# Optimization experiments

Hardware: AMD Instinct MI355X
Metric: run time of the kernel (lower is better)

## Reference

```python
import jax, jax.numpy as jnp
import numpy as np
import math

BH, L, D = 128, 1024, 64  # batch*heads, maxLen, head_dim
MASK_VALUE = -1000000.0


def setup_inputs() -> dict:
    key = jax.random.key(0)
    kq, kk, kv, kl = jax.random.split(key, 4)
    return {
        "queries": jax.random.normal(kq, (BH, L, D), dtype=jnp.float32),
        "keys": jax.random.normal(kk, (BH, L, D), dtype=jnp.float32),
        "values": jax.random.normal(kv, (BH, L, D), dtype=jnp.float32),
        "valid_lens": jax.random.randint(kl, (BH,), 0, L, dtype=jnp.int32),
    }


def reference(queries, keys, values, valid_lens):
    d = queries.shape[-1]
    # scores: [BH, Lq, Lk]
    scores = jnp.einsum("bqd,bkd->bqk", queries, keys) / math.sqrt(d)
    # key-padding mask: position k valid iff k < valid_len[b]
    mask = jnp.arange(scores.shape[-1])[None, None, :] < valid_lens[:, None, None]
    scores = jnp.where(mask, scores, MASK_VALUE)
    attn = jax.nn.softmax(scores, axis=-1)
    # dropout is identity at inference (Keras Dropout, training=False)
    return jnp.einsum("bqk,bkd->bqd", attn, values)
```

## Files before the change

### kernel.cpp

```cpp
#include <hip/hip_runtime.h>
#include <hip/hip_bf16.h>

#define BH 128
#define L 1024
#define D 64
#define MASK_VALUE -1000000.0f
#define KVBLK 64
#define M0 12.0f

typedef __attribute__((ext_vector_type(8))) __bf16 bf16x8;
typedef __attribute__((ext_vector_type(4))) float f32x4;
typedef __attribute__((ext_vector_type(4))) unsigned int u32x4;

__device__ __forceinline__ unsigned short f2bf(float f) {
    __bf16 h = (__bf16)f;
    return __builtin_bit_cast(unsigned short, h);
}

__device__ __forceinline__ unsigned cvt_pk(float lo, float hi) {
    unsigned r;
    asm("v_cvt_pk_bf16_f32 %0, %1, %2" : "=v"(r) : "v"(lo), "v"(hi));
    return r;
}

__device__ __forceinline__ float exp2_asm(float x) {
    float r; asm("v_exp_f32 %0, %1" : "=v"(r) : "v"(x)); return r;
}

__device__ __forceinline__ f32x4 mfma16(bf16x8 a, bf16x8 b, f32x4 c) {
    return __builtin_amdgcn_mfma_f32_16x16x32_bf16(a, b, c, 0, 0, 0);
}

__device__ __forceinline__ bf16x8 ldsfrag(const unsigned char* base, int row, int colbytes) {
    const u32x4* p = (const u32x4*)(base + row * 128 + (colbytes ^ ((row & 7) << 4)));
    return __builtin_bit_cast(bf16x8, *p);
}

__device__ __forceinline__ int sigma_k(int k) {
    return (k & 0x23) | ((k & 0x0C) << 1) | ((k & 0x10) >> 2);
}

__device__ __forceinline__ int nkt_of(int valid) {
    return (valid == 0) ? (L / KVBLK) : ((valid + KVBLK - 1) >> 6);
}

__global__ void sort_heads(const int* __restrict__ vlen, int* __restrict__ perm) {
    const int j  = threadIdx.x;
    const int nk = nkt_of(vlen[j]);
    int r = 0;
    for (int i = 0; i < BH; ++i) {
        const int nki = nkt_of(vlen[i]);
        if (nki > nk || (nki == nk && i < j)) ++r;
    }
    perm[r] = j;
}

__global__ __launch_bounds__(512)
void attn_kernel(const float* __restrict__ Q, const float* __restrict__ K,
                 const float* __restrict__ V, const int* __restrict__ vlen,
                 const int* __restrict__ perm, float* __restrict__ Out) {
    __shared__ __align__(16) unsigned char Kl[2][64 * 128];
    __shared__ __align__(16) unsigned char Vl[2][64 * 128];

    const int tid  = threadIdx.x;
    const int lane = tid & 63;
    const int wid  = tid >> 6;

    const int bid  = blockIdx.x;
    const int xcd  = bid & 7;
    const int slot = bid >> 3;
    const int c    = slot & 31;
    const int rr   = slot >> 5;
    const int idx  = (rr & 1) ? (rr * 32 + 31 - c) : (rr * 32 + c);
    const int l    = idx >> 3;
    const int qt   = idx & 7;
    const int head = perm[(l << 3) | xcd];

    const int valid = vlen[head];
    const int nkt   = nkt_of(valid);
    const float MASKV = (valid == 0) ? -M0 : MASK_VALUE;

    const float* Qh = Q + (size_t)head * L * D;
    const float* Kh = K + (size_t)head * L * D;
    const float* Vh = V + (size_t)head * L * D;
    float*       Oh = Out + (size_t)head * L * D;

    const int qrow0 = qt * 128 + wid * 16;
    const int q16   = lane & 15;
    const int hi    = lane >> 4;
    const int c8    = hi * 8;

    const float QSCALE = 0.125f * 1.44269504088896f;
    bf16x8 qf[2];
#pragma unroll
    for (int kk = 0; kk < 2; ++kk) {
        const float* qp = Qh + (qrow0 + q16) * D + kk * 32 + c8;
        f32x4 a = *(const f32x4*)qp;
        f32x4 b = *(const f32x4*)(qp + 4);
        u32x4 w;
        w[0] = cvt_pk(a[0] * QSCALE, a[1] * QSCALE);
        w[1] = cvt_pk(a[2] * QSCALE, a[3] * QSCALE);
        w[2] = cvt_pk(b[0] * QSCALE, b[1] * QSCALE);
        w[3] = cvt_pk(b[2] * QSCALE, b[3] * QSCALE);
        qf[kk] = __builtin_bit_cast(bf16x8, w);
    }

    const int skr = tid >> 3;
    const int skc = (tid & 7) * 8;
    const int svk2 = (tid & 31) * 2;
    const int svd4 = (tid >> 5) * 4;
    const int svcb = sigma_k(svk2) * 2;

    f32x4 rk0, rk1;
    f32x4 rva, rvb;

    auto load_regs = [&](int kt) {
        const float* kp = Kh + (size_t)(kt * KVBLK + skr) * D + skc;
        rk0 = *(const f32x4*)kp;
        rk1 = *(const f32x4*)(kp + 4);
        const float* vp = Vh + (size_t)(kt * KVBLK + svk2) * D + svd4;
        rva = *(const f32x4*)vp;
        rvb = *(const f32x4*)(vp + D);
    };

    auto write_lds = [&](int buf) {
        unsigned char* kb = Kl[buf];
        u32x4 w;
        w[0] = cvt_pk(rk0[0], rk0[1]);
        w[1] = cvt_pk(rk0[2], rk0[3]);
        w[2] = cvt_pk(rk1[0], rk1[1]);
        w[3] = cvt_pk(rk1[2], rk1[3]);
        *(u32x4*)(kb + skr * 128 + ((skc * 2) ^ ((skr & 7) << 4))) = w;
        unsigned char* vb = Vl[buf];
#pragma unroll
        for (int j = 0; j < 4; ++j) {
            int row = svd4 + j;
            *(unsigned*)(vb + row * 128 + (svcb ^ ((row & 7) << 4))) = cvt_pk(rva[j], rvb[j]);
        }
    };

    f32x4 o[4];
#pragma unroll
    for (int t = 0; t < 4; ++t) { o[t][0] = 0.f; o[t][1] = 0.f; o[t][2] = 0.f; o[t][3] = 0.f; }
    float l_part = 0.f;

    load_regs(0);
    write_lds(0);
    __syncthreads();

    for (int kt = 0; kt < nkt; ++kt) {
        const int  cur      = kt & 1;
        const bool has_next = (kt + 1 < nkt);
        if (has_next) load_regs(kt + 1);

        f32x4 s[4];
        __builtin_amdgcn_s_setprio(1);
#pragma unroll
        for (int st = 0; st < 4; ++st) {
            bf16x8 kf0 = ldsfrag(Kl[cur], st * 16 + q16, c8 * 2);
            bf16x8 kf1 = ldsfrag(Kl[cur], st * 16 + q16, (32 + c8) * 2);
            f32x4 acc; acc[0] = -M0; acc[1] = -M0; acc[2] = -M0; acc[3] = -M0;
            acc = mfma16(kf0, qf[0], acc);
            acc = mfma16(kf1, qf[1], acc);
            s[st] = acc;
        }
        __builtin_amdgcn_s_setprio(0);

        if ((kt + 1) * KVBLK > valid) {
            const int kb = kt * KVBLK + hi * 4;
#pragma unroll
            for (int st = 0; st < 4; ++st)
#pragma unroll
                for (int r = 0; r < 4; ++r)
                    if (kb + st * 16 + r >= valid) s[st][r] = MASKV;
        }

#pragma unroll
        for (int st = 0; st < 4; ++st)
#pragma unroll
            for (int r = 0; r < 4; ++r)
                s[st][r] = exp2_asm(s[st][r]);

        u32x4 pw0, pw1;
        pw0[0] = cvt_pk(s[0][0], s[0][1]); pw0[1] = cvt_pk(s[0][2], s[0][3]);
        pw0[2] = cvt_pk(s[1][0], s[1][1]); pw0[3] = cvt_pk(s[1][2], s[1][3]);
        pw1[0] = cvt_pk(s[2][0], s[2][1]); pw1[1] = cvt_pk(s[2][2], s[2][3]);
        pw1[2] = cvt_pk(s[3][0], s[3][1]); pw1[3] = cvt_pk(s[3][2], s[3][3]);
        bf16x8 pf0 = __builtin_bit_cast(bf16x8, pw0);
        bf16x8 pf1 = __builtin_bit_cast(bf16x8, pw1);

        __builtin_amdgcn_s_setprio(1);
#pragma unroll
        for (int t = 0; t < 4; ++t) {
            bf16x8 vf0 = ldsfrag(Vl[cur], t * 16 + q16, c8 * 2);
            bf16x8 vf1 = ldsfrag(Vl[cur], t * 16 + q16, (32 + c8) * 2);
            o[t] = mfma16(pf0, vf0, o[t]);
            o[t] = mfma16(pf1, vf1, o[t]);
        }
        __builtin_amdgcn_s_setprio(0);

        float u0 = (s[0][0] + s[0][1]) + (s[0][2] + s[0][3]);
        float u1 = (s[1][0] + s[1][1]) + (s[1][2] + s[1][3]);
        float u2 = (s[2][0] + s[2][1]) + (s[2][2] + s[2][3]);
        float u3 = (s[3][0] + s[3][1]) + (s[3][2] + s[3][3]);
        l_part += (u0 + u1) + (u2 + u3);

        if (has_next) write_lds((kt + 1) & 1);
        __syncthreads();
    }

    float lsum = l_part;
    lsum += __shfl_xor(lsum, 16);
    lsum += __shfl_xor(lsum, 32);
    float linv = 1.0f / lsum;
    float r0 = __shfl(linv, hi * 4 + 0);
    float r1 = __shfl(linv, hi * 4 + 1);
    float r2 = __shfl(linv, hi * 4 + 2);
    float r3 = __shfl(linv, hi * 4 + 3);
#pragma unroll
    for (int t = 0; t < 4; ++t) {
        const int d = t * 16 + q16;
        Oh[(size_t)(qrow0 + hi * 4 + 0) * D + d] = o[t][0] * r0;
        Oh[(size_t)(qrow0 + hi * 4 + 1) * D + d] = o[t][1] * r1;
        Oh[(size_t)(qrow0 + hi * 4 + 2) * D + d] = o[t][2] * r2;
        Oh[(size_t)(qrow0 + hi * 4 + 3) * D + d] = o[t][3] * r3;
    }
}

extern "C" void kernel_launch(void* const* d_in, const int* in_sizes, int n_in,
                              void* d_out, int out_size, void* d_ws, size_t ws_size,
                              hipStream_t stream) {
    const float* Q    = (const float*)d_in[0];
    const float* K    = (const float*)d_in[1];
    const float* V    = (const float*)d_in[2];
    const int*   vlen = (const int*)d_in[3];
    float*       Out  = (float*)d_out;
    int*         perm = (int*)d_ws;

    sort_heads<<<1, 128, 0, stream>>>(vlen, perm);
    dim3 grid(BH * (L / 128));
    attn_kernel<<<grid, 512, 0, stream>>>(Q, K, V, vlen, perm, Out);
}
```

Measured before the change: 43.95 us.

## Software-pipeline QK of next KV tile with PV of current tile

Splits the K and V load and store paths and restructures the main loop so the QK^T MFMAs and softmax for tile t+1 are issued around the PV MFMAs for tile t. K is prefetched two tiles ahead and V one tile ahead, with a prologue that computes the first score tile. The goal is to overlap exp/pack VALU work and LDS traffic with matrix-core work inside each wave. The cost is a second __syncthreads per iteration and a longer-lived score/P register state, which may raise register pressure. It also removes an unused helper.

```diff
diff --git a/kernel.cpp b/kernel.cpp
--- a/kernel.cpp
+++ b/kernel.cpp
@@ -11,11 +11,6 @@
 typedef __attribute__((ext_vector_type(8))) __bf16 bf16x8;
 typedef __attribute__((ext_vector_type(4))) float f32x4;
 typedef __attribute__((ext_vector_type(4))) unsigned int u32x4;
-
-__device__ __forceinline__ unsigned short f2bf(float f) {
-    __bf16 h = (__bf16)f;
-    return __builtin_bit_cast(unsigned short, h);
-}
 
 __device__ __forceinline__ unsigned cvt_pk(float lo, float hi) {
     unsigned r;
@@ -114,16 +109,17 @@
     f32x4 rk0, rk1;
     f32x4 rva, rvb;
 
-    auto load_regs = [&](int kt) {
+    auto load_k = [&](int kt) {
         const float* kp = Kh + (size_t)(kt * KVBLK + skr) * D + skc;
         rk0 = *(const f32x4*)kp;
         rk1 = *(const f32x4*)(kp + 4);
+    };
+    auto load_v = [&](int kt) {
         const float* vp = Vh + (size_t)(kt * KVBLK + svk2) * D + svd4;
         rva = *(const f32x4*)vp;
         rvb = *(const f32x4*)(vp + D);
     };
-
-    auto write_lds = [&](int buf) {
+    auto write_k = [&](int buf) {
         unsigned char* kb = Kl[buf];
         u32x4 w;
         w[0] = cvt_pk(rk0[0], rk0[1]);
@@ -131,6 +127,8 @@
         w[2] = cvt_pk(rk1[0], rk1[1]);
         w[3] = cvt_pk(rk1[2], rk1[3]);
         *(u32x4*)(kb + skr * 128 + ((skc * 2) ^ ((skr & 7) << 4))) = w;
+    };
+    auto write_v = [&](int buf) {
         unsigned char* vb = Vl[buf];
 #pragma unroll
         for (int j = 0; j < 4; ++j) {
@@ -144,28 +142,23 @@
     for (int t = 0; t < 4; ++t) { o[t][0] = 0.f; o[t][1] = 0.f; o[t][2] = 0.f; o[t][3] = 0.f; }
     float l_part = 0.f;
 
-    load_regs(0);
-    write_lds(0);
-    __syncthreads();
-
-    for (int kt = 0; kt < nkt; ++kt) {
-        const int  cur      = kt & 1;
-        const bool has_next = (kt + 1 < nkt);
-        if (has_next) load_regs(kt + 1);
-
-        f32x4 s[4];
+    f32x4 s[4];
+    bf16x8 pf0, pf1;
+
+    auto qk_tile = [&](int buf) {
         __builtin_amdgcn_s_setprio(1);
 #pragma unroll
         for (int st = 0; st < 4; ++st) {
-            bf16x8 kf0 = ldsfrag(Kl[cur], st * 16 + q16, c8 * 2);
-            bf16x8 kf1 = ldsfrag(Kl[cur], st * 16 + q16, (32 + c8) * 2);
+            bf16x8 kf0 = ldsfrag(Kl[buf], st * 16 + q16, c8 * 2);
+            bf16x8 kf1 = ldsfrag(Kl[buf], st * 16 + q16, (32 + c8) * 2);
             f32x4 acc; acc[0] = -M0; acc[1] = -M0; acc[2] = -M0; acc[3] = -M0;
             acc = mfma16(kf0, qf[0], acc);
             acc = mfma16(kf1, qf[1], acc);
             s[st] = acc;
         }
         __builtin_amdgcn_s_setprio(0);
-
+    };
+    auto mask_tile = [&](int kt) {
         if ((kt + 1) * KVBLK > valid) {
             const int kb = kt * KVBLK + hi * 4;
 #pragma unroll
@@ -174,38 +167,63 @@
                 for (int r = 0; r < 4; ++r)
                     if (kb + st * 16 + r >= valid) s[st][r] = MASKV;
         }
-
+    };
+    auto sm_pack = [&]() {
 #pragma unroll
         for (int st = 0; st < 4; ++st)
 #pragma unroll
             for (int r = 0; r < 4; ++r)
                 s[st][r] = exp2_asm(s[st][r]);
-
+        float u0 = (s[0][0] + s[0][1]) + (s[0][2] + s[0][3]);
+        float u1 = (s[1][0] + s[1][1]) + (s[1][2] + s[1][3]);
+        float u2 = (s[2][0] + s[2][1]) + (s[2][2] + s[2][3]);
+        float u3 = (s[3][0] + s[3][1]) + (s[3][2] + s[3][3]);
+        l_part += (u0 + u1) + (u2 + u3);
         u32x4 pw0, pw1;
         pw0[0] = cvt_pk(s[0][0], s[0][1]); pw0[1] = cvt_pk(s[0][2], s[0][3]);
         pw0[2] = cvt_pk(s[1][0], s[1][1]); pw0[3] = cvt_pk(s[1][2], s[1][3]);
         pw1[0] = cvt_pk(s[2][0], s[2][1]); pw1[1] = cvt_pk(s[2][2], s[2][3]);
         pw1[2] = cvt_pk(s[3][0], s[3][1]); pw1[3] = cvt_pk(s[3][2], s[3][3]);
-        bf16x8 pf0 = __builtin_bit_cast(bf16x8, pw0);
-        bf16x8 pf1 = __builtin_bit_cast(bf16x8, pw1);
-
+        pf0 = __builtin_bit_cast(bf16x8, pw0);
+        pf1 = __builtin_bit_cast(bf16x8, pw1);
+    };
+    auto pv_tile = [&](int buf) {
         __builtin_amdgcn_s_setprio(1);
 #pragma unroll
         for (int t = 0; t < 4; ++t) {
-            bf16x8 vf0 = ldsfrag(Vl[cur], t * 16 + q16, c8 * 2);
-            bf16x8 vf1 = ldsfrag(Vl[cur], t * 16 + q16, (32 + c8) * 2);
+            bf16x8 vf0 = ldsfrag(Vl[buf], t * 16 + q16, c8 * 2);
+            bf16x8 vf1 = ldsfrag(Vl[buf], t * 16 + q16, (32 + c8) * 2);
             o[t] = mfma16(pf0, vf0, o[t]);
             o[t] = mfma16(pf1, vf1, o[t]);
         }
         __builtin_amdgcn_s_setprio(0);
-
-        float u0 = (s[0][0] + s[0][1]) + (s[0][2] + s[0][3]);
-        float u1 = (s[1][0] + s[1][1]) + (s[1][2] + s[1][3]);
-        float u2 = (s[2][0] + s[2][1]) + (s[2][2] + s[2][3]);
-        float u3 = (s[3][0] + s[3][1]) + (s[3][2] + s[3][3]);
-        l_part += (u0 + u1) + (u2 + u3);
-
-        if (has_next) write_lds((kt + 1) & 1);
+    };
+
+    load_k(0); load_v(0);
+    write_k(0); write_v(0);
+    if (nkt > 1) { load_k(1); write_k(1); }
+    __syncthreads();
+
+    qk_tile(0);
+    mask_tile(0);
+    sm_pack();
+
+    for (int t = 0; t < nkt; ++t) {
+        const bool h1 = (t + 1 < nkt);
+        const bool h2 = (t + 2 < nkt);
+        if (h2) load_k(t + 2);
+        if (h1) {
+            load_v(t + 1);
+            qk_tile((t + 1) & 1);
+        }
+        __syncthreads();
+        pv_tile(t & 1);
+        if (h2) write_k(t & 1);
+        if (h1) {
+            write_v((t + 1) & 1);
+            mask_tile(t + 1);
+            sm_pack();
+        }
         __syncthreads();
     }
 
```

New measurement: 49.73 us. 13.2% more time.
